# Optimization experiments

Measured on AMD Instinct MI355X. Metric: run time of the kernel, lower is better.

## Reference

```python
import jax, jax.numpy as jnp
import numpy as np

LN_EPS = 1e-5

def setup_inputs() -> dict:
    key = jax.random.key(0)
    ks = jax.random.split(key, 8)
    B, N, C = 8, 16384, 256
    x = jax.random.normal(ks[0], (B, N, C), dtype=jnp.float32)
    time_decay = jax.random.normal(ks[1], (C,), dtype=jnp.float32) * 0.1
    s = 1.0 / np.sqrt(C)
    W_k = jax.random.normal(ks[2], (C, C), dtype=jnp.float32) * s
    W_v = jax.random.normal(ks[3], (C, C), dtype=jnp.float32) * s
    W_r = jax.random.normal(ks[4], (C, C), dtype=jnp.float32) * s
    W_o = jax.random.normal(ks[5], (C, C), dtype=jnp.float32) * s
    ln_w = jnp.ones((C,), dtype=jnp.float32)
    ln_b = jnp.zeros((C,), dtype=jnp.float32)
    return {"x": x, "time_decay": time_decay, "W_k": W_k, "W_v": W_v,
            "W_r": W_r, "W_o": W_o, "ln_w": ln_w, "ln_b": ln_b}

def _layernorm(x, w, b):
    mu = jnp.mean(x, axis=-1, keepdims=True)
    var = jnp.mean(jnp.square(x - mu), axis=-1, keepdims=True)
    return (x - mu) * jax.lax.rsqrt(var + LN_EPS) * w + b

def reference(x, time_decay, W_k, W_v, W_r, W_o, ln_w, ln_b):
    # x: (B, N, C)
    xn = _layernorm(x, ln_w, ln_b)
    k = jnp.einsum('bnc,dc->bnd', xn, W_k)
    v = jnp.einsum('bnc,dc->bnd', xn, W_v)
    r = jax.nn.sigmoid(jnp.einsum('bnc,dc->bnd', xn, W_r))
    decay = jnp.exp(-jax.nn.relu(time_decay))  # (C,)

    def step(state, k_t):
        state = state * decay + k_t  # (B, C)
        return state, state

    k_tm = jnp.swapaxes(k, 0, 1)  # (N, B, C) time-major for scan
    init = jnp.zeros(k.shape[::2], dtype=x.dtype)  # (B, C)
    _, states = jax.lax.scan(step, init, k_tm)
    states = jnp.swapaxes(states, 0, 1)  # (B, N, C)
    y = r * (states + v)
    y = jnp.einsum('bnc,dc->bnd', y, W_o)
    return y
```

## Files before the change

kernel.cpp:

```cpp
#include <hip/hip_runtime.h>
#include <hip/hip_bf16.h>
#include <stdint.h>


typedef __attribute__((ext_vector_type(8))) short short8;
typedef __attribute__((ext_vector_type(4))) float f32x4;

static __device__ __forceinline__ unsigned short f2bf(float f) {
  __hip_bfloat16 h = __float2bfloat16(f);
  return *reinterpret_cast<unsigned short*>(&h);
}
static __device__ __forceinline__ float bf2f(unsigned short u) {
  unsigned int v = ((unsigned int)u) << 16;
  float f;
  __builtin_memcpy(&f, &v, 4);
  return f;
}

__global__ void ln_kernel(const float* __restrict__ x,
                          const float* __restrict__ w,
                          const float* __restrict__ b,
                          unsigned short* __restrict__ xn) {
  const int wv = threadIdx.x >> 6;
  const int ln = threadIdx.x & 63;
  const size_t row = (size_t)blockIdx.x * 4 + wv;
  const float4 v = reinterpret_cast<const float4*>(x)[row * 64 + ln];
  float s  = v.x + v.y + v.z + v.w;
  float sq = v.x * v.x + v.y * v.y + v.z * v.z + v.w * v.w;
#pragma unroll
  for (int off = 32; off; off >>= 1) {
    s  += __shfl_xor(s, off, 64);
    sq += __shfl_xor(sq, off, 64);
  }
  const float mu  = s * (1.0f / 256.0f);
  const float var = sq * (1.0f / 256.0f) - mu * mu;
  const float rs  = rsqrtf(var + 1e-5f);
  const float4 w4 = reinterpret_cast<const float4*>(w)[ln];
  const float4 b4 = reinterpret_cast<const float4*>(b)[ln];
  ushort4 o;
  o.x = f2bf((v.x - mu) * rs * w4.x + b4.x);
  o.y = f2bf((v.y - mu) * rs * w4.y + b4.y);
  o.z = f2bf((v.z - mu) * rs * w4.z + b4.z);
  o.w = f2bf((v.w - mu) * rs * w4.w + b4.w);
  reinterpret_cast<ushort4*>(xn)[row * 64 + ln] = o;
}

__global__ void cvt_weights(const float* __restrict__ Wk,
                            const float* __restrict__ Wv,
                            const float* __restrict__ Wr,
                            const float* __restrict__ Wo,
                            unsigned short* __restrict__ Wkvr,
                            unsigned short* __restrict__ Wob) {
  const int idx = blockIdx.x * 256 + threadIdx.x;
  if (idx < 768 * 256) {
    const int r = idx >> 8;
    const int c = idx & 255;
    const float* src = (r < 256) ? Wk : ((r < 512) ? Wv : Wr);
    Wkvr[idx] = f2bf(src[(r & 255) * 256 + c]);
  } else {
    const int j = idx - 768 * 256;
    Wob[j] = f2bf(Wo[j]);
  }
}

template <int EPI>
__global__ void gemm_bt(const unsigned short* __restrict__ A,
                        const unsigned short* __restrict__ Bt,
                        unsigned short* __restrict__ kbuf,
                        unsigned short* __restrict__ vbuf,
                        unsigned short* __restrict__ rbuf,
                        float* __restrict__ outf) {
  constexpr int K = 256;
  __shared__ unsigned short Als[128][64];
  __shared__ unsigned short Bls[128][64];

  const int tid = threadIdx.x;
  const int wv = tid >> 6;
  const int ln = tid & 63;
  const int bm0 = blockIdx.x * 128;
  const int bn0 = blockIdx.y * 128;
  const int lq = ln >> 4;
  const int lm = ln & 15;

  f32x4 acc[4][4];
#pragma unroll
  for (int i = 0; i < 4; ++i)
#pragma unroll
    for (int j = 0; j < 4; ++j) acc[i][j] = (f32x4){0.f, 0.f, 0.f, 0.f};

  const int m0w = (wv >> 1) * 64;
  const int n0w = (wv & 1) * 64;

  const int srow = ln >> 3;
  const int schunk = (ln & 7) ^ srow;

  for (int kk0 = 0; kk0 < K; kk0 += 64) {
#pragma unroll
    for (int i = 0; i < 4; ++i) {
      const int rr = wv * 32 + i * 8;
      const unsigned short* gA = A + (size_t)(bm0 + rr + srow) * K + kk0 + schunk * 8;
      __builtin_amdgcn_global_load_lds(
          (const __attribute__((address_space(1))) void*)gA,
          (__attribute__((address_space(3))) void*)&Als[rr][0], 16, 0, 0);
      const unsigned short* gB = Bt + (size_t)(bn0 + rr + srow) * K + kk0 + schunk * 8;
      __builtin_amdgcn_global_load_lds(
          (const __attribute__((address_space(1))) void*)gB,
          (__attribute__((address_space(3))) void*)&Bls[rr][0], 16, 0, 0);
    }
    __syncthreads();
#pragma unroll
    for (int kk = 0; kk < 64; kk += 32) {
      short8 af[4], bfr[4];
      const int chunk = (kk >> 3) + lq;
#pragma unroll
      for (int t = 0; t < 4; ++t) {
        const int rowa = m0w + t * 16 + lm;
        af[t] = *reinterpret_cast<const short8*>(&Als[rowa][(chunk ^ (rowa & 7)) * 8]);
        const int rowb = n0w + t * 16 + lm;
        bfr[t] = *reinterpret_cast<const short8*>(&Bls[rowb][(chunk ^ (rowb & 7)) * 8]);
      }
#pragma unroll
      for (int mt = 0; mt < 4; ++mt)
#pragma unroll
        for (int nt = 0; nt < 4; ++nt)
          acc[mt][nt] = __builtin_amdgcn_mfma_f32_16x16x32_bf16(
              af[mt], bfr[nt], acc[mt][nt], 0, 0, 0);
    }
    __syncthreads();
  }

#pragma unroll
  for (int mt = 0; mt < 4; ++mt) {
#pragma unroll
    for (int nt = 0; nt < 4; ++nt) {
      const int n_g = bn0 + n0w + nt * 16 + lm;
      const int m_base = bm0 + m0w + mt * 16 + lq * 4;
      if (EPI == 0) {
        const int bufi = n_g >> 8;
        const int col = n_g & 255;
        unsigned short* dst = (bufi == 0) ? kbuf : ((bufi == 1) ? vbuf : rbuf);
#pragma unroll
        for (int r = 0; r < 4; ++r) {
          float val = acc[mt][nt][r];
          if (bufi == 2) val = 1.0f / (1.0f + __expf(-val));
          dst[(size_t)(m_base + r) * 256 + col] = f2bf(val);
        }
      } else {
#pragma unroll
        for (int r = 0; r < 4; ++r)
          outf[(size_t)(m_base + r) * 256 + n_g] = acc[mt][nt][r];
      }
    }
  }
}

__global__ void scan_carry(const unsigned short* __restrict__ k,
                           const float* __restrict__ td,
                           float* __restrict__ carry) {
  const int bch = blockIdx.x;
  const int c = threadIdx.x;
  const float d = expf(-fmaxf(td[c], 0.0f));
  const unsigned short* kp = k + (size_t)bch * 128 * 256 + c;
  float s = 0.0f;
#pragma unroll 8
  for (int i = 0; i < 128; ++i) s = s * d + bf2f(kp[(size_t)i * 256]);
  carry[(size_t)bch * 256 + c] = s;
}

__global__ void scan_chunks(float* __restrict__ carry,
                            const float* __restrict__ td) {
  const int b = blockIdx.x;
  const int c = threadIdx.x;
  const float relu_td = fmaxf(td[c], 0.0f);
  const float dL = expf(-relu_td * 128.0f);
  float s = 0.0f;
  for (int j = 0; j < 128; ++j) {
    const size_t idx = ((size_t)b * 128 + j) * 256 + c;
    const float cj = carry[idx];
    carry[idx] = s;
    s = dL * s + cj;
  }
}

__global__ void scan_final(unsigned short* __restrict__ k,
                           const unsigned short* __restrict__ v,
                           const unsigned short* __restrict__ r,
                           const float* __restrict__ carryin,
                           const float* __restrict__ td) {
  const int bch = blockIdx.x;
  const int c = threadIdx.x;
  const float d = expf(-fmaxf(td[c], 0.0f));
  const size_t base = (size_t)bch * 128 * 256 + c;
  float s = carryin[(size_t)bch * 256 + c];
#pragma unroll 4
  for (int i = 0; i < 128; ++i) {
    const size_t off = base + (size_t)i * 256;
    s = s * d + bf2f(k[off]);
    const float y = bf2f(r[off]) * (s + bf2f(v[off]));
    k[off] = f2bf(y);
  }
}

extern "C" void kernel_launch(void* const* d_in, const int* in_sizes, int n_in,
                              void* d_out, int out_size, void* d_ws, size_t ws_size,
                              hipStream_t stream) {
  const float* x   = (const float*)d_in[0];
  const float* td  = (const float*)d_in[1];
  const float* Wk  = (const float*)d_in[2];
  const float* Wv  = (const float*)d_in[3];
  const float* Wr  = (const float*)d_in[4];
  const float* Wo  = (const float*)d_in[5];
  const float* lnw = (const float*)d_in[6];
  const float* lnb = (const float*)d_in[7];
  float* out = (float*)d_out;

  const int Bsz = 8, C = 256;
  const size_t M = 131072;

  char* ws = (char*)d_ws;
  size_t off = 0;
  auto alloc = [&](size_t bytes) -> char* {
    char* p = ws + off;
    off += (bytes + 255) & ~(size_t)255;
    return p;
  };
  unsigned short* xn   = (unsigned short*)alloc(M * C * 2);
  unsigned short* kbuf = (unsigned short*)alloc(M * C * 2);
  unsigned short* vbuf = (unsigned short*)alloc(M * C * 2);
  unsigned short* rbuf = (unsigned short*)alloc(M * C * 2);
  unsigned short* Wkvr = (unsigned short*)alloc(768 * 256 * 2);
  unsigned short* Wob  = (unsigned short*)alloc(256 * 256 * 2);
  float* carry = (float*)alloc((size_t)Bsz * 128 * C * 4);
  (void)ws_size; (void)in_sizes; (void)n_in; (void)out_size;

  cvt_weights<<<dim3(1024), dim3(256), 0, stream>>>(Wk, Wv, Wr, Wo, Wkvr, Wob);
  ln_kernel<<<dim3((unsigned)(M / 4)), dim3(256), 0, stream>>>(x, lnw, lnb, xn);
  gemm_bt<0><<<dim3((unsigned)(M / 128), 6), dim3(256), 0, stream>>>(
      xn, Wkvr, kbuf, vbuf, rbuf, nullptr);
  scan_carry<<<dim3(Bsz * 128), dim3(256), 0, stream>>>(kbuf, td, carry);
  scan_chunks<<<dim3(Bsz), dim3(256), 0, stream>>>(carry, td);
  scan_final<<<dim3(Bsz * 128), dim3(256), 0, stream>>>(kbuf, vbuf, rbuf, carry, td);
  gemm_bt<1><<<dim3((unsigned)(M / 128), 2), dim3(256), 0, stream>>>(
      kbuf, Wob, nullptr, nullptr, nullptr, out);
}
```

Baseline: 446.1 us.

## Vectorize GEMM epilogue stores and scan kernels, reorder GEMM block mapping

Swaps the MFMA operand order so each lane holds four consecutive output columns, which lets the GEMM epilogue write packed ushort4/float4 stores instead of strided scalar stores. The 2D grid is flattened so consecutive blocks share an M tile across all N tiles, which should improve L2 reuse of the A rows. The scan kernels are rewritten so each thread handles 8 channels with 16-byte vector loads, and chunk length drops from 128 to 64, giving 256 chunks per batch and a larger carry buffer. The cost is a longer serial chunk-carry pass and fewer, heavier scan blocks.

```diff
diff --git a/kernel.cpp b/kernel.cpp
--- a/kernel.cpp
+++ b/kernel.cpp
@@ -63,7 +63,7 @@
   }
 }
 
-template <int EPI>
+template <int EPI, int NY>
 __global__ void gemm_bt(const unsigned short* __restrict__ A,
                         const unsigned short* __restrict__ Bt,
                         unsigned short* __restrict__ kbuf,
@@ -77,8 +77,9 @@
   const int tid = threadIdx.x;
   const int wv = tid >> 6;
   const int ln = tid & 63;
-  const int bm0 = blockIdx.x * 128;
-  const int bn0 = blockIdx.y * 128;
+  const int bid = blockIdx.x;
+  const int bm0 = (bid / NY) * 128;
+  const int bn0 = (bid % NY) * 128;
   const int lq = ln >> 4;
   const int lm = ln & 15;
 
@@ -124,31 +125,32 @@
 #pragma unroll
         for (int nt = 0; nt < 4; ++nt)
           acc[mt][nt] = __builtin_amdgcn_mfma_f32_16x16x32_bf16(
-              af[mt], bfr[nt], acc[mt][nt], 0, 0, 0);
+              bfr[nt], af[mt], acc[mt][nt], 0, 0, 0);
     }
     __syncthreads();
   }
 
 #pragma unroll
   for (int mt = 0; mt < 4; ++mt) {
+    const int m_g = bm0 + m0w + mt * 16 + lm;
 #pragma unroll
     for (int nt = 0; nt < 4; ++nt) {
-      const int n_g = bn0 + n0w + nt * 16 + lm;
-      const int m_base = bm0 + m0w + mt * 16 + lq * 4;
+      const int n_base = bn0 + n0w + nt * 16 + lq * 4;
+      f32x4 a = acc[mt][nt];
       if (EPI == 0) {
-        const int bufi = n_g >> 8;
-        const int col = n_g & 255;
+        const int bufi = n_base >> 8;
+        const int col = n_base & 255;
         unsigned short* dst = (bufi == 0) ? kbuf : ((bufi == 1) ? vbuf : rbuf);
-#pragma unroll
-        for (int r = 0; r < 4; ++r) {
-          float val = acc[mt][nt][r];
-          if (bufi == 2) val = 1.0f / (1.0f + __expf(-val));
-          dst[(size_t)(m_base + r) * 256 + col] = f2bf(val);
+        if (bufi == 2) {
+#pragma unroll
+          for (int r = 0; r < 4; ++r) a[r] = 1.0f / (1.0f + __expf(-a[r]));
         }
+        ushort4 pk;
+        pk.x = f2bf(a[0]); pk.y = f2bf(a[1]); pk.z = f2bf(a[2]); pk.w = f2bf(a[3]);
+        *reinterpret_cast<ushort4*>(&dst[(size_t)m_g * 256 + col]) = pk;
       } else {
-#pragma unroll
-        for (int r = 0; r < 4; ++r)
-          outf[(size_t)(m_base + r) * 256 + n_g] = acc[mt][nt][r];
+        float4 o = make_float4(a[0], a[1], a[2], a[3]);
+        *reinterpret_cast<float4*>(&outf[(size_t)m_g * 256 + n_base]) = o;
       }
     }
   }
@@ -157,28 +159,44 @@
 __global__ void scan_carry(const unsigned short* __restrict__ k,
                            const float* __restrict__ td,
                            float* __restrict__ carry) {
-  const int bch = blockIdx.x;
-  const int c = threadIdx.x;
-  const float d = expf(-fmaxf(td[c], 0.0f));
-  const unsigned short* kp = k + (size_t)bch * 128 * 256 + c;
-  float s = 0.0f;
-#pragma unroll 8
-  for (int i = 0; i < 128; ++i) s = s * d + bf2f(kp[(size_t)i * 256]);
-  carry[(size_t)bch * 256 + c] = s;
+  const int lane32 = threadIdx.x & 31;
+  const int sub = threadIdx.x >> 5;
+  const int bch = blockIdx.x * 8 + sub;
+  const int c0 = lane32 * 8;
+  float d[8], s[8];
+#pragma unroll
+  for (int j = 0; j < 8; ++j) {
+    d[j] = expf(-fmaxf(td[c0 + j], 0.0f));
+    s[j] = 0.0f;
+  }
+  const unsigned short* kp = k + (size_t)bch * 64 * 256 + c0;
+#pragma unroll 4
+  for (int i = 0; i < 64; ++i) {
+    short8 kv = *reinterpret_cast<const short8*>(kp + (size_t)i * 256);
+#pragma unroll
+    for (int j = 0; j < 8; ++j) s[j] = s[j] * d[j] + bf2f((unsigned short)kv[j]);
+  }
+  float4* cp = reinterpret_cast<float4*>(carry + (size_t)bch * 256 + c0);
+  cp[0] = make_float4(s[0], s[1], s[2], s[3]);
+  cp[1] = make_float4(s[4], s[5], s[6], s[7]);
 }
 
 __global__ void scan_chunks(float* __restrict__ carry,
                             const float* __restrict__ td) {
   const int b = blockIdx.x;
   const int c = threadIdx.x;
-  const float relu_td = fmaxf(td[c], 0.0f);
-  const float dL = expf(-relu_td * 128.0f);
+  const float dL = expf(-fmaxf(td[c], 0.0f) * 64.0f);
   float s = 0.0f;
-  for (int j = 0; j < 128; ++j) {
-    const size_t idx = ((size_t)b * 128 + j) * 256 + c;
-    const float cj = carry[idx];
-    carry[idx] = s;
-    s = dL * s + cj;
+  float* base = carry + (size_t)b * 256 * 256 + c;
+  for (int j0 = 0; j0 < 256; j0 += 8) {
+    float buf[8];
+#pragma unroll
+    for (int t = 0; t < 8; ++t) buf[t] = base[(size_t)(j0 + t) * 256];
+#pragma unroll
+    for (int t = 0; t < 8; ++t) {
+      base[(size_t)(j0 + t) * 256] = s;
+      s = dL * s + buf[t];
+    }
   }
 }
 
@@ -187,17 +205,32 @@
                            const unsigned short* __restrict__ r,
                            const float* __restrict__ carryin,
                            const float* __restrict__ td) {
-  const int bch = blockIdx.x;
-  const int c = threadIdx.x;
-  const float d = expf(-fmaxf(td[c], 0.0f));
-  const size_t base = (size_t)bch * 128 * 256 + c;
-  float s = carryin[(size_t)bch * 256 + c];
-#pragma unroll 4
-  for (int i = 0; i < 128; ++i) {
+  const int lane32 = threadIdx.x & 31;
+  const int sub = threadIdx.x >> 5;
+  const int bch = blockIdx.x * 8 + sub;
+  const int c0 = lane32 * 8;
+  float d[8], s[8];
+  const float4* ci = reinterpret_cast<const float4*>(carryin + (size_t)bch * 256 + c0);
+  float4 c0v = ci[0], c1v = ci[1];
+  s[0] = c0v.x; s[1] = c0v.y; s[2] = c0v.z; s[3] = c0v.w;
+  s[4] = c1v.x; s[5] = c1v.y; s[6] = c1v.z; s[7] = c1v.w;
+#pragma unroll
+  for (int j = 0; j < 8; ++j) d[j] = expf(-fmaxf(td[c0 + j], 0.0f));
+  const size_t base = (size_t)bch * 64 * 256 + c0;
+#pragma unroll 2
+  for (int i = 0; i < 64; ++i) {
     const size_t off = base + (size_t)i * 256;
-    s = s * d + bf2f(k[off]);
-    const float y = bf2f(r[off]) * (s + bf2f(v[off]));
-    k[off] = f2bf(y);
+    short8 kv = *reinterpret_cast<const short8*>(k + off);
+    short8 vv = *reinterpret_cast<const short8*>(v + off);
+    short8 rv = *reinterpret_cast<const short8*>(r + off);
+    short8 y;
+#pragma unroll
+    for (int j = 0; j < 8; ++j) {
+      s[j] = s[j] * d[j] + bf2f((unsigned short)kv[j]);
+      const float yj = bf2f((unsigned short)rv[j]) * (s[j] + bf2f((unsigned short)vv[j]));
+      y[j] = (short)f2bf(yj);
+    }
+    *reinterpret_cast<short8*>(k + off) = y;
   }
 }
 
@@ -230,16 +263,16 @@
   unsigned short* rbuf = (unsigned short*)alloc(M * C * 2);
   unsigned short* Wkvr = (unsigned short*)alloc(768 * 256 * 2);
   unsigned short* Wob  = (unsigned short*)alloc(256 * 256 * 2);
-  float* carry = (float*)alloc((size_t)Bsz * 128 * C * 4);
+  float* carry = (float*)alloc((size_t)Bsz * 256 * C * 4);
   (void)ws_size; (void)in_sizes; (void)n_in; (void)out_size;
 
   cvt_weights<<<dim3(1024), dim3(256), 0, stream>>>(Wk, Wv, Wr, Wo, Wkvr, Wob);
   ln_kernel<<<dim3((unsigned)(M / 4)), dim3(256), 0, stream>>>(x, lnw, lnb, xn);
-  gemm_bt<0><<<dim3((unsigned)(M / 128), 6), dim3(256), 0, stream>>>(
+  gemm_bt<0, 6><<<dim3(1024 * 6), dim3(256), 0, stream>>>(
       xn, Wkvr, kbuf, vbuf, rbuf, nullptr);
-  scan_carry<<<dim3(Bsz * 128), dim3(256), 0, stream>>>(kbuf, td, carry);
+  scan_carry<<<dim3(256), dim3(256), 0, stream>>>(kbuf, td, carry);
   scan_chunks<<<dim3(Bsz), dim3(256), 0, stream>>>(carry, td);
-  scan_final<<<dim3(Bsz * 128), dim3(256), 0, stream>>>(kbuf, vbuf, rbuf, carry, td);
-  gemm_bt<1><<<dim3((unsigned)(M / 128), 2), dim3(256), 0, stream>>>(
+  scan_final<<<dim3(256), dim3(256), 0, stream>>>(kbuf, vbuf, rbuf, carry, td);
+  gemm_bt<1, 2><<<dim3(1024 * 2), dim3(256), 0, stream>>>(
       kbuf, Wob, nullptr, nullptr, nullptr, out);
 }
```

After: 440.3 us. About the same (-1.3%).
